# Kernel optimization log

Hardware: AMD Instinct MI355X
Metric: run time of the kernel (lower is better)

## Reference

```python
import jax, jax.numpy as jnp
import numpy as np

B, S, E = 4, 2048, 512
H = 8          # 'layers' = number of heads
DK, DV = 64, 64
DK_H, DV_H = DK // H, DV // H  # = 8 each


def setup_inputs() -> dict:
    key = jax.random.key(0)
    ks = jax.random.split(key, 8)
    scale = 1.0 / np.sqrt(E)
    return {
        "query": jax.random.normal(ks[0], (B, S, E), jnp.float32),
        "key": jax.random.normal(ks[1], (B, S, E), jnp.float32),
        "value": jax.random.normal(ks[2], (B, S, E), jnp.float32),
        "padding_mask": jnp.ones((B, S, S), dtype=bool),
        "decoder_mask": 1,
        # stacked per-head projection weights (nn.Linear, bias=False)
        "Wq": jax.random.normal(ks[3], (H, E, DK_H), jnp.float32) * scale,
        "Wk": jax.random.normal(ks[4], (H, E, DK_H), jnp.float32) * scale,
        "Wv": jax.random.normal(ks[5], (H, E, DV_H), jnp.float32) * scale,
        # output projection: Linear(dV -> embed_size) with bias
        "Wo": jax.random.normal(ks[6], (DV, E), jnp.float32) * (1.0 / np.sqrt(DV)),
        "bo": jax.random.normal(ks[7], (E,), jnp.float32) * 0.01,
    }


def reference(query, key, value, padding_mask, decoder_mask, Wq, Wk, Wv, Wo, bo):
    # Batched over all heads at once (same math as the per-head Python loop).
    Q = jnp.einsum("bse,hed->bhsd", query, Wq)   # [B,H,S,dk_h]
    K = jnp.einsum("bse,hed->bhsd", key, Wk)
    V = jnp.einsum("bse,hed->bhsd", value, Wv)
    s = jnp.einsum("bhsd,bhtd->bhst", Q, K)      # [B,H,S,S] raw scores
    if decoder_mask:
        # faithful to: where(tril(scores)==0.0, -inf, scores)
        s = jnp.where(jnp.tril(s) == 0.0, -jnp.inf, s)
    # masked_fill(~padding_mask, -inf), broadcast over heads
    s = jnp.where(padding_mask[:, None, :, :], s, -jnp.inf)
    # note: scaling happens AFTER masking in the original (-inf stays -inf)
    s = s / jnp.sqrt(jnp.float32(DK_H))
    a = jax.nn.softmax(s, axis=-1)
    # dropout in eval mode -> identity
    o = jnp.einsum("bhst,bhtd->bhsd", a, V)      # [B,H,S,dv_h]
    o = o.transpose(0, 2, 1, 3).reshape(o.shape[0], o.shape[2], H * DV_H)  # concat heads
    return o @ Wo + bo                            # output projection (dropout = identity)
```

## Files before the change

### kernel.cpp

```cpp
#include <hip/hip_runtime.h>

#define BB 4
#define SS 2048
#define EE 512
#define HH 8
#define DHH 8
#define DVV 64

#define NEG (-1e30f)

__global__ __launch_bounds__(256)
void proj_kernel(const float* __restrict__ q, const float* __restrict__ k,
                 const float* __restrict__ v,
                 const float* __restrict__ Wq, const float* __restrict__ Wk,
                 const float* __restrict__ Wv,
                 float* __restrict__ Qp, float* __restrict__ Kp,
                 float* __restrict__ Vp)
{
  const float* x; const float* W; float* outp;
  if (blockIdx.y == 0)      { x = q; W = Wq; outp = Qp; }
  else if (blockIdx.y == 1) { x = k; W = Wk; outp = Kp; }
  else                      { x = v; W = Wv; outp = Vp; }

  __shared__ float Xs[64][68];
  __shared__ float Ws[64][68];

  int t = threadIdx.x;
  int row0 = blockIdx.x * 64;
  int tr = t >> 4;
  int tc = t & 15;

  float acc[4][4];
  #pragma unroll
  for (int i = 0; i < 4; i++)
    #pragma unroll
    for (int j = 0; j < 4; j++) acc[i][j] = 0.f;

  for (int kt = 0; kt < EE/64; kt++) {
    __syncthreads();
    {
      int row = t >> 2;
      #pragma unroll
      for (int it = 0; it < 4; it++) {
        int kq = 4*it + (t & 3);
        float4 vv = *(const float4*)(x + (size_t)(row0+row)*EE + kt*64 + 4*kq);
        Xs[4*kq+0][row] = vv.x;
        Xs[4*kq+1][row] = vv.y;
        Xs[4*kq+2][row] = vv.z;
        Xs[4*kq+3][row] = vv.w;
      }
    }
    #pragma unroll
    for (int it = 0; it < 4; it++) {
      int lin = t + 256*it;
      int kk  = lin >> 4;
      int rem = lin & 15;
      int h   = rem >> 1;
      int dq  = rem & 1;
      float4 vv = *(const float4*)(W + (size_t)h*EE*DHH + (size_t)(kt*64+kk)*DHH + dq*4);
      *(float4*)&Ws[kk][h*8 + dq*4] = vv;
    }
    __syncthreads();

    #pragma unroll 8
    for (int kk = 0; kk < 64; kk++) {
      float4 a = *(const float4*)&Xs[kk][4*tr];
      float4 bq = *(const float4*)&Ws[kk][4*tc];
      float av[4] = {a.x, a.y, a.z, a.w};
      float bv[4] = {bq.x, bq.y, bq.z, bq.w};
      #pragma unroll
      for (int i = 0; i < 4; i++)
        #pragma unroll
        for (int j = 0; j < 4; j++) acc[i][j] += av[i] * bv[j];
    }
  }

  int h = tc >> 1, dbase = (tc & 1) * 4;
  #pragma unroll
  for (int i = 0; i < 4; i++) {
    int row = row0 + 4*tr + i;
    int b = row >> 11, s = row & (SS - 1);
    float4 vv; vv.x = acc[i][0]; vv.y = acc[i][1]; vv.z = acc[i][2]; vv.w = acc[i][3];
    *(float4*)(outp + (((size_t)b*HH + h)*SS + s)*DHH + dbase) = vv;
  }
}

__global__ __launch_bounds__(256, 2)
void attn_kernel(const float* __restrict__ Qp, const float* __restrict__ Kp,
                 const float* __restrict__ Vp, float* __restrict__ O)
{
  int bx = blockIdx.x, h = blockIdx.y, b = blockIdx.z;
  const float* Qh = Qp + (((size_t)b*HH + h)*SS)*DHH;
  const float* Kh = Kp + (((size_t)b*HH + h)*SS)*DHH;
  const float* Vh = Vp + (((size_t)b*HH + h)*SS)*DHH;

  __shared__ float Ks[128*DHH];
  __shared__ float Vs[128*DHH];
  __shared__ float Ps[4*64*10];

  int t = threadIdx.x;
  int r2  = t & 31;
  int tcw = t >> 5;
  const float scale = 0.35355339059327373f;

  for (int pass = 0; pass < 2; pass++) {
    int qb = (pass == 0) ? bx : (31 - bx);
    int row0t = qb*64 + 2*r2;

    float qreg[2][8];
    #pragma unroll
    for (int i = 0; i < 2; i++) {
      const float* qp = Qh + (size_t)(row0t + i) * DHH;
      *(float4*)&qreg[i][0] = *(const float4*)qp;
      *(float4*)&qreg[i][4] = *(const float4*)(qp + 4);
    }

    float m[2] = {NEG, NEG};
    float l[2] = {0.f, 0.f};
    float o[2][8];
    #pragma unroll
    for (int i = 0; i < 2; i++)
      #pragma unroll
      for (int d = 0; d < 8; d++) o[i][d] = 0.f;

    int ktd = qb >> 1;
    for (int kt = 0; kt <= ktd; kt++) {
      __syncthreads();
      ((float4*)Ks)[t] = ((const float4*)(Kh + (size_t)kt*128*DHH))[t];
      ((float4*)Vs)[t] = ((const float4*)(Vh + (size_t)kt*128*DHH))[t];
      __syncthreads();

      if (kt < ktd) {
        float sc[16][2];
        float smax[2] = {NEG, NEG};
        #pragma unroll
        for (int j = 0; j < 16; j++) {
          int c = tcw + 8*j;
          float4 k0 = *(const float4*)&Ks[c*8];
          float4 k1 = *(const float4*)&Ks[c*8 + 4];
          #pragma unroll
          for (int i = 0; i < 2; i++) {
            float s = qreg[i][0]*k0.x + qreg[i][1]*k0.y + qreg[i][2]*k0.z + qreg[i][3]*k0.w
                    + qreg[i][4]*k1.x + qreg[i][5]*k1.y + qreg[i][6]*k1.z + qreg[i][7]*k1.w;
            s *= scale;
            sc[j][i] = s;
            smax[i] = fmaxf(smax[i], s);
          }
        }
        #pragma unroll
        for (int i = 0; i < 2; i++) {
          float mnew = fmaxf(m[i], smax[i]);
          float alpha = __expf(m[i] - mnew);
          l[i] *= alpha;
          #pragma unroll
          for (int d = 0; d < 8; d++) o[i][d] *= alpha;
          m[i] = mnew;
        }
        #pragma unroll
        for (int j = 0; j < 16; j++) {
          int c = tcw + 8*j;
          float4 v0 = *(const float4*)&Vs[c*8];
          float4 v1 = *(const float4*)&Vs[c*8 + 4];
          #pragma unroll
          for (int i = 0; i < 2; i++) {
            float p = __expf(sc[j][i] - m[i]);
            l[i] += p;
            o[i][0] += p*v0.x; o[i][1] += p*v0.y; o[i][2] += p*v0.z; o[i][3] += p*v0.w;
            o[i][4] += p*v1.x; o[i][5] += p*v1.y; o[i][6] += p*v1.z; o[i][7] += p*v1.w;
          }
        }
      } else {
        for (int j0 = 0; j0 < 16; j0 += 8) {
          if (kt*128 + tcw + 8*j0 > row0t + 1) break;

          float sc[8][2];
          float smax[2] = {NEG, NEG};
          #pragma unroll
          for (int j = 0; j < 8; j++) {
            int c = tcw + 8*(j0 + j);
            int cg = kt*128 + c;
            float4 k0 = *(const float4*)&Ks[c*8];
            float4 k1 = *(const float4*)&Ks[c*8 + 4];
            #pragma unroll
            for (int i = 0; i < 2; i++) {
              float s = qreg[i][0]*k0.x + qreg[i][1]*k0.y + qreg[i][2]*k0.z + qreg[i][3]*k0.w
                      + qreg[i][4]*k1.x + qreg[i][5]*k1.y + qreg[i][6]*k1.z + qreg[i][7]*k1.w;
              s *= scale;
              s = (cg > row0t + i) ? NEG : s;
              sc[j][i] = s;
              smax[i] = fmaxf(smax[i], s);
            }
          }
          float mexp[2];
          #pragma unroll
          for (int i = 0; i < 2; i++) {
            float mnew = fmaxf(m[i], smax[i]);
            float alpha = __expf(m[i] - mnew);
            l[i] *= alpha;
            #pragma unroll
            for (int d = 0; d < 8; d++) o[i][d] *= alpha;
            m[i] = mnew;
            mexp[i] = (mnew > -1e29f) ? mnew : 1e30f;
          }
          #pragma unroll
          for (int j = 0; j < 8; j++) {
            int c = tcw + 8*(j0 + j);
            float4 v0 = *(const float4*)&Vs[c*8];
            float4 v1 = *(const float4*)&Vs[c*8 + 4];
            #pragma unroll
            for (int i = 0; i < 2; i++) {
              float p = __expf(sc[j][i] - mexp[i]);
              l[i] += p;
              o[i][0] += p*v0.x; o[i][1] += p*v0.y; o[i][2] += p*v0.z; o[i][3] += p*v0.w;
              o[i][4] += p*v1.x; o[i][5] += p*v1.y; o[i][6] += p*v1.z; o[i][7] += p*v1.w;
            }
          }
        }
      }
    }

    #pragma unroll
    for (int i = 0; i < 2; i++) {
      float mo = __shfl_xor(m[i], 32);
      float lo = __shfl_xor(l[i], 32);
      float mm = fmaxf(m[i], mo);
      float a1 = __expf(m[i] - mm);
      float a2 = __expf(mo - mm);
      l[i] = l[i]*a1 + lo*a2;
      #pragma unroll
      for (int d = 0; d < 8; d++) {
        float od = __shfl_xor(o[i][d], 32);
        o[i][d] = o[i][d]*a1 + od*a2;
      }
      m[i] = mm;
    }

    int w = t >> 6;
    if ((t & 32) == 0) {
      #pragma unroll
      for (int i = 0; i < 2; i++) {
        float* ps = &Ps[(w*64 + 2*r2 + i)*10];
        ps[0] = m[i]; ps[1] = l[i];
        #pragma unroll
        for (int d = 0; d < 8; d++) ps[2+d] = o[i][d];
      }
    }
    __syncthreads();

    if (t < 64) {
      float M = NEG, L = 0.f, O8[8] = {0,0,0,0,0,0,0,0};
      #pragma unroll
      for (int ww = 0; ww < 4; ww++) {
        const float* ps = &Ps[(ww*64 + t)*10];
        float mo = ps[0], lo = ps[1];
        float mm = fmaxf(M, mo);
        float a1 = __expf(M - mm);
        float a2 = __expf(mo - mm);
        L = L*a1 + lo*a2;
        #pragma unroll
        for (int d = 0; d < 8; d++) O8[d] = O8[d]*a1 + ps[2+d]*a2;
        M = mm;
      }
      float inv = 1.0f / L;
      int qrow = qb*64 + t;
      float* dst = O + ((size_t)b*SS + qrow)*DVV + h*DHH;
      float4 w0, w1;
      w0.x = O8[0]*inv; w0.y = O8[1]*inv; w0.z = O8[2]*inv; w0.w = O8[3]*inv;
      w1.x = O8[4]*inv; w1.y = O8[5]*inv; w1.z = O8[6]*inv; w1.w = O8[7]*inv;
      *(float4*)dst = w0;
      *(float4*)(dst + 4) = w1;
    }
    __syncthreads();
  }
}

__global__ __launch_bounds__(256)
void outproj_kernel(const float* __restrict__ Oin, const float* __restrict__ Wo,
                    const float* __restrict__ bo, float* __restrict__ out)
{
  __shared__ float Os[64][68];
  int t = threadIdx.x;
  int row0 = blockIdx.x * 64;
  int col0 = blockIdx.y * 128;

  {
    int row = t >> 2;
    #pragma unroll
    for (int it = 0; it < 4; it++) {
      int kq = 4*it + (t & 3);
      float4 vv = *(const float4*)(Oin + (size_t)(row0+row)*DVV + 4*kq);
      Os[4*kq+0][row] = vv.x;
      Os[4*kq+1][row] = vv.y;
      Os[4*kq+2][row] = vv.z;
      Os[4*kq+3][row] = vv.w;
    }
  }
  __syncthreads();

  int rg = t >> 5;
  int tc = t & 31;
  const float* wp = Wo + col0 + 4*tc;
  float4 b4 = *(const float4*)(bo + col0 + 4*tc);

  float acc[8][4];
  #pragma unroll
  for (int r = 0; r < 8; r++) {
    acc[r][0] = b4.x; acc[r][1] = b4.y; acc[r][2] = b4.z; acc[r][3] = b4.w;
  }

  #pragma unroll 8
  for (int k = 0; k < DVV; k++) {
    float4 w = *(const float4*)(wp + (size_t)k*EE);
    float xr[8];
    *(float4*)&xr[0] = *(const float4*)&Os[k][8*rg];
    *(float4*)&xr[4] = *(const float4*)&Os[k][8*rg + 4];
    #pragma unroll
    for (int r = 0; r < 8; r++) {
      acc[r][0] += xr[r]*w.x;
      acc[r][1] += xr[r]*w.y;
      acc[r][2] += xr[r]*w.z;
      acc[r][3] += xr[r]*w.w;
    }
  }

  #pragma unroll
  for (int r = 0; r < 8; r++) {
    int row = row0 + 8*rg + r;
    float4 vv; vv.x = acc[r][0]; vv.y = acc[r][1]; vv.z = acc[r][2]; vv.w = acc[r][3];
    *(float4*)(out + (size_t)row*EE + col0 + 4*tc) = vv;
  }
}

extern "C" void kernel_launch(void* const* d_in, const int* in_sizes, int n_in,
                              void* d_out, int out_size, void* d_ws, size_t ws_size,
                              hipStream_t stream) {
  const void* qkv[3] = {nullptr, nullptr, nullptr};
  const void* Wlist[4] = {nullptr, nullptr, nullptr, nullptr};
  const void* bo = nullptr;
  int nqkv = 0, nw = 0;
  for (int i = 0; i < n_in; i++) {
    int sz = in_sizes[i];
    if (sz == BB*SS*EE)            { if (nqkv < 3) qkv[nqkv] = d_in[i]; nqkv++; }
    else if (sz == HH*EE*DHH)      { if (nw < 4) Wlist[nw] = d_in[i]; nw++; }
    else if (sz == EE)             { bo = d_in[i]; }
  }
  float* out = (float*)d_out;

  float* Qp = (float*)d_ws;
  float* Kp = Qp + (size_t)BB*HH*SS*DHH;
  float* Vp = Kp + (size_t)BB*HH*SS*DHH;
  float* O  = Vp + (size_t)BB*HH*SS*DHH;

  dim3 gA(BB*SS/64, 3, 1);
  proj_kernel<<<gA, 256, 0, stream>>>((const float*)qkv[0], (const float*)qkv[1],
                                      (const float*)qkv[2],
                                      (const float*)Wlist[0], (const float*)Wlist[1],
                                      (const float*)Wlist[2], Qp, Kp, Vp);

  dim3 gB(16, HH, BB);
  attn_kernel<<<gB, 256, 0, stream>>>(Qp, Kp, Vp, O);

  dim3 gC(BB*SS/64, EE/128, 1);
  outproj_kernel<<<gC, 256, 0, stream>>>(O, (const float*)Wlist[3],
                                         (const float*)bo, out);
}
```

Before: 237.1 us.

## Rewrite QKV projection as per-row register GEMV without shared memory

Replaces the shared-memory tiled 64x64 projection GEMM with a one-wavefront-per-block kernel. Each lane handles one input row and 32 output columns, reading X rows directly with prefetched float4 loads and reading weights from global memory (broadcast across lanes). This removes LDS staging and barriers. In exchange, X row loads are strided across lanes (uncoalesced), and there is more per-lane weight traffic, which now relies on the caches.

New measurement: 352.7 us. 1.49x slower.

```diff
diff --git a/kernel.cpp b/kernel.cpp
--- a/kernel.cpp
+++ b/kernel.cpp
@@ -9,7 +9,7 @@
 
 #define NEG (-1e30f)
 
-__global__ __launch_bounds__(256)
+__global__ __launch_bounds__(64)
 void proj_kernel(const float* __restrict__ q, const float* __restrict__ k,
                  const float* __restrict__ v,
                  const float* __restrict__ Wq, const float* __restrict__ Wk,
@@ -22,66 +22,48 @@
   else if (blockIdx.y == 1) { x = k; W = Wk; outp = Kp; }
   else                      { x = v; W = Wv; outp = Vp; }
 
-  __shared__ float Xs[64][68];
-  __shared__ float Ws[64][68];
-
-  int t = threadIdx.x;
-  int row0 = blockIdx.x * 64;
-  int tr = t >> 4;
-  int tc = t & 15;
-
-  float acc[4][4];
-  #pragma unroll
-  for (int i = 0; i < 4; i++)
-    #pragma unroll
-    for (int j = 0; j < 4; j++) acc[i][j] = 0.f;
-
-  for (int kt = 0; kt < EE/64; kt++) {
-    __syncthreads();
-    {
-      int row = t >> 2;
-      #pragma unroll
-      for (int it = 0; it < 4; it++) {
-        int kq = 4*it + (t & 3);
-        float4 vv = *(const float4*)(x + (size_t)(row0+row)*EE + kt*64 + 4*kq);
-        Xs[4*kq+0][row] = vv.x;
-        Xs[4*kq+1][row] = vv.y;
-        Xs[4*kq+2][row] = vv.z;
-        Xs[4*kq+3][row] = vv.w;
-      }
-    }
-    #pragma unroll
-    for (int it = 0; it < 4; it++) {
-      int lin = t + 256*it;
-      int kk  = lin >> 4;
-      int rem = lin & 15;
-      int h   = rem >> 1;
-      int dq  = rem & 1;
-      float4 vv = *(const float4*)(W + (size_t)h*EE*DHH + (size_t)(kt*64+kk)*DHH + dq*4);
-      *(float4*)&Ws[kk][h*8 + dq*4] = vv;
-    }
-    __syncthreads();
-
-    #pragma unroll 8
-    for (int kk = 0; kk < 64; kk++) {
-      float4 a = *(const float4*)&Xs[kk][4*tr];
-      float4 bq = *(const float4*)&Ws[kk][4*tc];
-      float av[4] = {a.x, a.y, a.z, a.w};
-      float bv[4] = {bq.x, bq.y, bq.z, bq.w};
-      #pragma unroll
-      for (int i = 0; i < 4; i++)
-        #pragma unroll
-        for (int j = 0; j < 4; j++) acc[i][j] += av[i] * bv[j];
-    }
-  }
-
-  int h = tc >> 1, dbase = (tc & 1) * 4;
-  #pragma unroll
-  for (int i = 0; i < 4; i++) {
-    int row = row0 + 4*tr + i;
-    int b = row >> 11, s = row & (SS - 1);
-    float4 vv; vv.x = acc[i][0]; vv.y = acc[i][1]; vv.z = acc[i][2]; vv.w = acc[i][3];
-    *(float4*)(outp + (((size_t)b*HH + h)*SS + s)*DHH + dbase) = vv;
+  int lane = threadIdx.x;
+  int row  = blockIdx.x * 32 + (lane & 31);
+  int half = lane >> 5;
+  const float* Xrow = x + (size_t)row * EE;
+
+  const float* Wp[8];
+  #pragma unroll
+  for (int j = 0; j < 8; j++) {
+    int col = half*32 + 4*j;
+    int h = col >> 3, d0 = col & 7;
+    Wp[j] = W + (size_t)h * EE * DHH + d0;
+  }
+
+  float acc[32];
+  #pragma unroll
+  for (int j = 0; j < 32; j++) acc[j] = 0.f;
+
+  float4 xv = *(const float4*)(Xrow);
+  for (int kk0 = 0; kk0 < EE; kk0 += 4) {
+    float4 xn;
+    if (kk0 + 4 < EE) xn = *(const float4*)(Xrow + kk0 + 4);
+    float xk[4] = {xv.x, xv.y, xv.z, xv.w};
+    #pragma unroll
+    for (int kk = 0; kk < 4; kk++) {
+      #pragma unroll
+      for (int j = 0; j < 8; j++) {
+        float4 w = *(const float4*)(Wp[j] + (size_t)(kk0 + kk) * DHH);
+        acc[4*j+0] += xk[kk] * w.x;
+        acc[4*j+1] += xk[kk] * w.y;
+        acc[4*j+2] += xk[kk] * w.z;
+        acc[4*j+3] += xk[kk] * w.w;
+      }
+    }
+    xv = xn;
+  }
+
+  int b = row >> 11, s = row & (SS - 1);
+  #pragma unroll
+  for (int j = 0; j < 8; j++) {
+    int col = half*32 + 4*j;
+    int h = col >> 3, d0 = col & 7;
+    *(float4*)(outp + (((size_t)b*HH + h)*SS + s)*DHH + d0) = *(float4*)&acc[4*j];
   }
 }
 
@@ -351,11 +333,11 @@
   float* Vp = Kp + (size_t)BB*HH*SS*DHH;
   float* O  = Vp + (size_t)BB*HH*SS*DHH;
 
-  dim3 gA(BB*SS/64, 3, 1);
-  proj_kernel<<<gA, 256, 0, stream>>>((const float*)qkv[0], (const float*)qkv[1],
-                                      (const float*)qkv[2],
-                                      (const float*)Wlist[0], (const float*)Wlist[1],
-                                      (const float*)Wlist[2], Qp, Kp, Vp);
+  dim3 gA(BB*SS/32, 3, 1);
+  proj_kernel<<<gA, 64, 0, stream>>>((const float*)qkv[0], (const float*)qkv[1],
+                                     (const float*)qkv[2],
+                                     (const float*)Wlist[0], (const float*)Wlist[1],
+                                     (const float*)Wlist[2], Qp, Kp, Vp);
 
   dim3 gB(16, HH, BB);
   attn_kernel<<<gB, 256, 0, stream>>>(Qp, Kp, Vp, O);
```
